# Performance work log

Measured on AMD Instinct MI355X. Metric: run time of the kernel, lower is better.

## Reference

```python
import jax, jax.numpy as jnp
import numpy as np
from jax import lax

B, C, W, H, K = 4, 32, 256, 256, 9
CENTER = K // 2
EXTEND = 1.0
EPS = 1e-5


def conv2d(x, w, b, stride=(1, 1), padding='SAME'):
    y = lax.conv_general_dilated(x, w, stride, padding,
                                 dimension_numbers=('NCHW', 'OIHW', 'NCHW'))
    return y + b[None, :, None, None]


def group_norm(x, scale, bias, groups):
    b, c, h, w = x.shape
    xg = x.reshape(b, groups, c // groups, h, w)
    mu = xg.mean(axis=(2, 3, 4), keepdims=True)
    var = xg.var(axis=(2, 3, 4), keepdims=True)
    xn = ((xg - mu) * lax.rsqrt(var + EPS)).reshape(b, c, h, w)
    return xn * scale[None, :, None, None] + bias[None, :, None, None]


def bilinear_sample(feat, py, px):
    # feat: (C, W, H); py, px: (W*K, H) pixel coords, already clamped in-range
    y0 = jnp.floor(py)
    x0 = jnp.floor(px)
    wy = py - y0
    wx = px - x0
    y0i = jnp.clip(y0, 0, W - 1).astype(jnp.int32)
    y1i = jnp.clip(y0 + 1, 0, W - 1).astype(jnp.int32)
    x0i = jnp.clip(x0, 0, H - 1).astype(jnp.int32)
    x1i = jnp.clip(x0 + 1, 0, H - 1).astype(jnp.int32)
    v00 = feat[:, y0i, x0i]
    v01 = feat[:, y0i, x1i]
    v10 = feat[:, y1i, x0i]
    v11 = feat[:, y1i, x1i]
    return (v00 * (1 - wy) * (1 - wx) + v01 * (1 - wy) * wx
            + v10 * wy * (1 - wx) + v11 * wy * wx)


def ds_conv(x, w_off, b_off, gn_off_scale, gn_off_bias, w_dsc, b_dsc, gn_scale, gn_bias):
    # offset branch: conv3x3 -> GroupNorm(K groups, 2K ch) -> tanh
    off = jnp.tanh(group_norm(conv2d(x, w_off, b_off), gn_off_scale, gn_off_bias, K))
    y_off = off[:, :K]  # (B, K, W, H); x-half of offsets unused when morph == 0
    # cumulative offset scan outward from center tap (center tap offset is 0)
    low = jnp.flip(jnp.cumsum(jnp.flip(y_off[:, :CENTER], 1), 1), 1)
    up = jnp.cumsum(y_off[:, CENTER + 1:], 1)
    y_cum = jnp.concatenate([low, jnp.zeros_like(y_off[:, :1]), up], axis=1)
    # coordinate maps (morph == 0: kernel spreads along x, offsets bend y)
    y_new = jnp.arange(W, dtype=x.dtype)[None, None, :, None] + y_cum * EXTEND
    x_new = (jnp.arange(H, dtype=x.dtype)[None, None, None, :]
             + jnp.linspace(-CENTER, CENTER, K, dtype=x.dtype)[None, :, None, None])
    x_new = jnp.broadcast_to(x_new, y_new.shape)
    gy = y_new.transpose(0, 2, 1, 3).reshape(-1, W * K, H)  # 'b k w h -> b (w k) h'
    gx = x_new.transpose(0, 2, 1, 3).reshape(-1, W * K, H)
    # normalize as torch grid_sample (align_corners=True) with clamp to [-1, 1]
    gy = jnp.clip(gy / W * 2 - 1, -1.0, 1.0)
    gx = jnp.clip(gx / H * 2 - 1, -1.0, 1.0)
    py = (gy + 1) * 0.5 * (W - 1)
    px = (gx + 1) * 0.5 * (H - 1)
    deformed = jax.vmap(bilinear_sample)(x, py, px)  # (B, C, W*K, H)
    out = conv2d(deformed, w_dsc, b_dsc, stride=(K, 1), padding='VALID')  # (B, C, W, H)
    out = group_norm(out, gn_scale, gn_bias, C // 4)
    return jax.nn.relu(out)


def setup_inputs() -> dict:
    key = jax.random.key(0)
    ks = jax.random.split(key, 3)
    return {
        'input': jax.random.normal(ks[0], (B, C, W, H), jnp.float32),
        'w_off': jax.random.normal(ks[1], (2 * K, C, 3, 3), jnp.float32) * 0.05,
        'b_off': jnp.zeros((2 * K,), jnp.float32),
        'gn_off_scale': jnp.ones((2 * K,), jnp.float32),
        'gn_off_bias': jnp.zeros((2 * K,), jnp.float32),
        'w_dsc': jax.random.normal(ks[2], (C, C, K, 1), jnp.float32) * 0.05,
        'b_dsc': jnp.zeros((C,), jnp.float32),
        'gn_scale': jnp.ones((C,), jnp.float32),
        'gn_bias': jnp.zeros((C,), jnp.float32),
    }


def reference(input, w_off, b_off, gn_off_scale, gn_off_bias, w_dsc, b_dsc, gn_scale, gn_bias):
    # in_channels == out_channels so input_adjust is Identity
    return ds_conv(input, w_off, b_off, gn_off_scale, gn_off_bias, w_dsc, b_dsc, gn_scale, gn_bias)
```

## Files before the change

### kernel.cpp

```cpp
#include <hip/hip_runtime.h>
#include <hip/hip_bf16.h>

#define BB 4
#define CC 32
#define WW 256
#define HH 256
#define WH (WW*HH)

typedef __attribute__((ext_vector_type(8))) short bf16x8;
typedef __attribute__((ext_vector_type(4))) short bf16x4;
typedef __attribute__((ext_vector_type(4))) float f32x4;

__device__ __forceinline__ short f2bf(float x) {
    union { float f; unsigned u; } a; a.f = x;
    unsigned r = (a.u + 0x7FFF + ((a.u >> 16) & 1)) >> 16;
    return (short)r;
}

__global__ void k0_init(const float* __restrict__ w_dsc, const float* __restrict__ w_off,
                        unsigned short* __restrict__ B3f, unsigned short* __restrict__ B8f,
                        unsigned short* __restrict__ B1f, unsigned short* __restrict__ B18f,
                        float* __restrict__ stats1, float* __restrict__ stats2) {
    int i = blockIdx.x * 256 + threadIdx.x;
    if (i < 8192) {
        int j = i & 7, l = (i >> 3) & 63, nt = (i >> 9) & 1, ch = i >> 10;
        int o = nt * 16 + (l & 15);
        int kl = ((l >> 4) << 3) | j;
        int tap = kl >> 2, cl = kl & 3;
        B3f[i] = (unsigned short)f2bf(w_dsc[(o * 32 + ch * 4 + cl) * 9 + tap]);
    } else if (i < 9216) {
        int e = i - 8192;
        int j = e & 7, l = (e >> 3) & 63, nt = e >> 9;
        int o = nt * 16 + (l & 15);
        int k8 = ((l >> 4) << 3) | j;
        B8f[e] = (unsigned short)f2bf(w_dsc[(o * 32 + k8) * 9 + 8]);
    } else if (i < 13312) {
        int e = i - 9216;
        int j = e & 7, l = (e >> 3) & 63, ch = e >> 9;
        int o = l & 15;
        int kl = ((l >> 4) << 3) | j;
        int tap = kl >> 2, cl = kl & 3;
        B1f[e] = (o < 10) ? (unsigned short)f2bf(w_off[(o * 32 + ch * 4 + cl) * 9 + tap]) : 0;
    } else if (i < 13824) {
        int e = i - 13312;
        int j = e & 7, l = (e >> 3) & 63;
        int o = l & 15;
        int k8 = ((l >> 4) << 3) | j;
        B18f[e] = (o < 10) ? (unsigned short)f2bf(w_off[(o * 32 + k8) * 9 + 8]) : 0;
    }
    if (i < 40) stats1[i] = 0.f;
    if (i < 64) stats2[i] = 0.f;
}

__global__ __launch_bounds__(256, 2) void k1_conv(
    const float* __restrict__ x, const unsigned short* __restrict__ B1f,
    const unsigned short* __restrict__ B18f, const float* __restrict__ b_off,
    float* __restrict__ off_buf, float* __restrict__ stats1) {
    __shared__ __align__(16) unsigned short tbf[8 * 4 * 136 * 4];
    __shared__ float scr[40];
    __shared__ __align__(16) short Apan[16 * 64 * 8];
    __shared__ __align__(16) short A8pan[16 * 64 * 8];

    const int b = blockIdx.z;
    const int w0 = blockIdx.y * 2;
    const int h0 = blockIdx.x * 128;
    const int p = threadIdx.x;
    const int lane = p & 63;
    const int wv = p >> 6;
    const int hl = p & 127;
    const int wi = p >> 7;
    const int mt = p >> 4;
    const int mrow = p & 15;

    const float* xb = x + (size_t)b * CC * WH;

#pragma unroll
    for (int u = 0; u < 5; ++u) {
        if (u < 4 || p < 64) {
            int s = p + u * 256;
            int g = s / 136;
            int rem = s - g * 136;
            int r = rem / 34;
            int k = rem - r * 34;
            int y = w0 - 1 + r;
            int g0 = h0 - 4 + (k << 2);
            f32x4 v0 = {0.f,0.f,0.f,0.f}, v1 = v0, v2 = v0, v3 = v0;
            if (y >= 0 && y < 256 && g0 >= 0 && g0 <= 252) {
                const float* bp2 = xb + y * 256 + g0;
                v0 = *(const f32x4*)(bp2 + (size_t)(g * 4 + 0) * WH);
                v1 = *(const f32x4*)(bp2 + (size_t)(g * 4 + 1) * WH);
                v2 = *(const f32x4*)(bp2 + (size_t)(g * 4 + 2) * WH);
                v3 = *(const f32x4*)(bp2 + (size_t)(g * 4 + 3) * WH);
            }
            int base = ((g * 4 + r) * 136 + (k << 2)) * 4;
#pragma unroll
            for (int i = 0; i < 4; ++i) {
                bf16x4 pv;
                pv[0] = f2bf(v0[i]); pv[1] = f2bf(v1[i]);
                pv[2] = f2bf(v2[i]); pv[3] = f2bf(v3[i]);
                *(bf16x4*)&tbf[base + i * 4] = pv;
            }
        }
    }

    bf16x8 Bf[8], B8g;
    {
        const bf16x8* bp = (const bf16x8*)B1f;
#pragma unroll
        for (int ch = 0; ch < 8; ++ch) Bf[ch] = bp[ch * 64 + lane];
        B8g = ((const bf16x8*)B18f)[lane];
    }

    f32x4 acc[4];
#pragma unroll
    for (int i = 0; i < 4; ++i) acc[i] = (f32x4){0.f, 0.f, 0.f, 0.f};

    __syncthreads();

#pragma unroll
    for (int ch = 0; ch < 8; ++ch) {
#pragma unroll
        for (int kg = 0; kg < 4; ++kg) {
            bf16x4 lo, hi;
            {
                int tap = kg * 2, dy = tap / 3, dx = tap - dy * 3;
                lo = *(const bf16x4*)&tbf[((ch * 4 + wi + dy) * 136 + hl + dx + 3) * 4];
            }
            {
                int tap = kg * 2 + 1, dy = tap / 3, dx = tap - dy * 3;
                hi = *(const bf16x4*)&tbf[((ch * 4 + wi + dy) * 136 + hl + dx + 3) * 4];
            }
            bf16x8 pv;
#pragma unroll
            for (int e = 0; e < 4; ++e) { pv[e] = lo[e]; pv[4 + e] = hi[e]; }
            *(bf16x8*)&Apan[mt * 512 + (kg * 16 + mrow) * 8] = pv;
        }
        {
            bf16x4 pv8 = *(const bf16x4*)&tbf[((ch * 4 + wi + 2) * 136 + hl + 5) * 4];
            *(bf16x4*)&A8pan[mt * 512 + ((ch >> 1) * 16 + mrow) * 8 + (ch & 1) * 4] = pv8;
        }
        __syncthreads();

#pragma unroll
        for (int i = 0; i < 4; ++i) {
            bf16x8 a = *(const bf16x8*)&Apan[((wv * 4 + i) * 64 + lane) * 8];
            acc[i] = __builtin_amdgcn_mfma_f32_16x16x32_bf16(a, Bf[ch], acc[i], 0, 0, 0);
        }
        __syncthreads();
    }
#pragma unroll
    for (int i = 0; i < 4; ++i) {
        bf16x8 a = *(const bf16x8*)&A8pan[((wv * 4 + i) * 64 + lane) * 8];
        acc[i] = __builtin_amdgcn_mfma_f32_16x16x32_bf16(a, B8g, acc[i], 0, 0, 0);
    }

    const int oc = lane & 15;
    float bias = (oc < 10) ? b_off[oc] : 0.f;
#pragma unroll
    for (int i = 0; i < 4; ++i)
#pragma unroll
        for (int r = 0; r < 4; ++r) acc[i][r] += bias;

    if (oc < 10) {
#pragma unroll
        for (int i = 0; i < 4; ++i) {
            int px = (wv * 4 + i) * 16 + (lane >> 4) * 4;
            size_t addr = (size_t)(b * 10 + oc) * WH +
                          (size_t)(w0 + (px >> 7)) * 256 + h0 + (px & 127);
            *(f32x4*)&off_buf[addr] = acc[i];
        }
    }

    float s = 0.f, q = 0.f;
#pragma unroll
    for (int i = 0; i < 4; ++i)
#pragma unroll
        for (int r = 0; r < 4; ++r) { float v = acc[i][r]; s += v; q += v * v; }
    s += __shfl_xor(s, 1, 64);  q += __shfl_xor(q, 1, 64);
    s += __shfl_xor(s, 16, 64); q += __shfl_xor(q, 16, 64);
    s += __shfl_xor(s, 32, 64); q += __shfl_xor(q, 32, 64);
    __syncthreads();
    if (lane < 10 && !(lane & 1)) {
        int g = lane >> 1;
        scr[(g * 2 + 0) * 4 + wv] = s;
        scr[(g * 2 + 1) * 4 + wv] = q;
    }
    __syncthreads();
    if (threadIdx.x < 10) {
        int g = threadIdx.x >> 1, which = threadIdx.x & 1;
        float sum = scr[(g * 2 + which) * 4 + 0] + scr[(g * 2 + which) * 4 + 1] +
                    scr[(g * 2 + which) * 4 + 2] + scr[(g * 2 + which) * 4 + 3];
        atomicAdd(&stats1[(b * 5 + g) * 2 + which], sum);
    }
}

__global__ __launch_bounds__(256, 2) void k3_sample(
    const float* __restrict__ xin, const float* __restrict__ off_buf,
    const float* __restrict__ stats1, const float* __restrict__ go_scale,
    const float* __restrict__ go_bias, const unsigned short* __restrict__ B3f,
    const unsigned short* __restrict__ B8f, const float* __restrict__ b_dsc,
    float* __restrict__ pre_out, float* __restrict__ stats2) {
    __shared__ float tile[4 * 14 * 96];
    __shared__ short Apan[16 * 64 * 8];
    __shared__ short A8pan[16 * 64 * 8];

    const int b = blockIdx.z;
    const int w0 = blockIdx.y * 4;
    const int h0 = blockIdx.x * 64;
    const int p = threadIdx.x;
    const int lane = p & 63;
    const int wv = p >> 6;
    const int h = h0 + (p & 63);
    const int w = w0 + (p >> 6);
    const int mt = p >> 4;
    const int mrow = p & 15;
    const int row0 = w0 - 5;
    const int col0 = h0 - 8;

    bf16x8 Bf[8][2], B8g[2];
    {
        const bf16x8* bp = (const bf16x8*)B3f;
#pragma unroll
        for (int ch = 0; ch < 8; ++ch) {
            Bf[ch][0] = bp[(ch * 2 + 0) * 64 + lane];
            Bf[ch][1] = bp[(ch * 2 + 1) * 64 + lane];
        }
        B8g[0] = ((const bf16x8*)B8f)[lane];
        B8g[1] = ((const bf16x8*)B8f)[64 + lane];
    }

    const float INV1 = 1.f / (2.f * WH);
    float t9[9];
    size_t obase = (size_t)b * 10 * WH + (size_t)w * 256 + h;
#pragma unroll
    for (int c = 0; c < 9; ++c) {
        float v = off_buf[obase + (size_t)c * WH];
        int g = c >> 1;
        float s1 = stats1[(b * 5 + g) * 2 + 0];
        float q1 = stats1[(b * 5 + g) * 2 + 1];
        float mean = s1 * INV1;
        float istd = rsqrtf(fmaf(q1, INV1, -(mean * mean)) + 1e-5f);
        v = (v - mean) * istd * go_scale[c] + go_bias[c];
        t9[c] = tanhf(v);
    }
    float ycum[9];
    ycum[3] = t9[3];
    ycum[2] = ycum[3] + t9[2];
    ycum[1] = ycum[2] + t9[1];
    ycum[0] = ycum[1] + t9[0];
    ycum[4] = 0.f;
    ycum[5] = t9[5];
    ycum[6] = ycum[5] + t9[6];
    ycum[7] = ycum[6] + t9[7];
    ycum[8] = ycum[7] + t9[8];

    f32x4 acc[4][2];
#pragma unroll
    for (int i = 0; i < 4; ++i) {
        acc[i][0] = (f32x4){0.f, 0.f, 0.f, 0.f};
        acc[i][1] = (f32x4){0.f, 0.f, 0.f, 0.f};
    }

    const float* xb = xin + (size_t)b * CC * WH;
    const float SC = 255.f / 256.f;

#pragma unroll
    for (int ch = 0; ch < 8; ++ch) {
        for (int t = threadIdx.x; t < 1064; t += 256) {
            int c = t / 266;
            int rem = t - c * 266;
            int r = rem / 19;
            int cf = rem - r * 19;
            int y = min(max(row0 + r, 0), 255);
            int g0 = col0 + (cf << 2);
            const float* src = xb + (size_t)(ch * 4 + c) * WH + y * 256;
            float4 val;
            if (g0 >= 0 && g0 <= 252) {
                val = *(const float4*)(src + g0);
            } else {
                val.x = src[min(max(g0, 0), 255)];
                val.y = src[min(max(g0 + 1, 0), 255)];
                val.z = src[min(max(g0 + 2, 0), 255)];
                val.w = src[min(max(g0 + 3, 0), 255)];
            }
            *(float4*)(tile + (c * 14 + r) * 96 + (cf << 2)) = val;
        }
        __syncthreads();

#pragma unroll
        for (int kg = 0; kg < 4; ++kg) {
            bf16x8 pv;
#pragma unroll
            for (int t = 0; t < 2; ++t) {
                int k = kg * 2 + t;
                float py = fminf(fmaxf(((float)w + ycum[k]) * SC, 0.f), 255.f);
                float pxc = fminf(fmaxf((float)(h + k - 4) * SC, 0.f), 255.f);
                float y0f = floorf(py), x0f = floorf(pxc);
                float wy = py - y0f, wx = pxc - x0f;
                int r0 = (int)y0f - row0;
                int r1 = min((int)y0f + 1, 255) - row0;
                int tc = (int)x0f - col0;
                float w00 = (1.f - wy) * (1.f - wx);
                float w01 = (1.f - wy) * wx;
                float w10 = wy * (1.f - wx);
                float w11 = wy * wx;
#pragma unroll
                for (int cl = 0; cl < 4; ++cl) {
                    const float* p0 = tile + (cl * 14 + r0) * 96 + tc;
                    const float* p1 = tile + (cl * 14 + r1) * 96 + tc;
                    float v = fmaf(w00, p0[0],
                              fmaf(w01, p0[1], fmaf(w10, p1[0], w11 * p1[1])));
                    pv[t * 4 + cl] = f2bf(v);
                }
            }
            *(bf16x8*)&Apan[mt * 512 + (kg * 16 + mrow) * 8] = pv;
        }
        {
            float py = fminf(fmaxf(((float)w + ycum[8]) * SC, 0.f), 255.f);
            float pxc = fminf(fmaxf((float)(h + 4) * SC, 0.f), 255.f);
            float y0f = floorf(py), x0f = floorf(pxc);
            float wy = py - y0f, wx = pxc - x0f;
            int r0 = (int)y0f - row0;
            int r1 = min((int)y0f + 1, 255) - row0;
            int tc = (int)x0f - col0;
            float w00 = (1.f - wy) * (1.f - wx);
            float w01 = (1.f - wy) * wx;
            float w10 = wy * (1.f - wx);
            float w11 = wy * wx;
            bf16x4 pv8;
#pragma unroll
            for (int cl = 0; cl < 4; ++cl) {
                const float* p0 = tile + (cl * 14 + r0) * 96 + tc;
                const float* p1 = tile + (cl * 14 + r1) * 96 + tc;
                float v = fmaf(w00, p0[0],
                          fmaf(w01, p0[1], fmaf(w10, p1[0], w11 * p1[1])));
                pv8[cl] = f2bf(v);
            }
            *(bf16x4*)&A8pan[mt * 512 + ((ch >> 1) * 16 + mrow) * 8 + (ch & 1) * 4] = pv8;
        }
        __syncthreads();

#pragma unroll
        for (int i = 0; i < 4; ++i) {
            bf16x8 a = *(const bf16x8*)&Apan[((wv * 4 + i) * 64 + lane) * 8];
            acc[i][0] = __builtin_amdgcn_mfma_f32_16x16x32_bf16(a, Bf[ch][0], acc[i][0], 0, 0, 0);
            acc[i][1] = __builtin_amdgcn_mfma_f32_16x16x32_bf16(a, Bf[ch][1], acc[i][1], 0, 0, 0);
        }
    }
#pragma unroll
    for (int i = 0; i < 4; ++i) {
        bf16x8 a = *(const bf16x8*)&A8pan[((wv * 4 + i) * 64 + lane) * 8];
        acc[i][0] = __builtin_amdgcn_mfma_f32_16x16x32_bf16(a, B8g[0], acc[i][0], 0, 0, 0);
        acc[i][1] = __builtin_amdgcn_mfma_f32_16x16x32_bf16(a, B8g[1], acc[i][1], 0, 0, 0);
    }

    const int oc0 = lane & 15;
    float bias0 = b_dsc[oc0];
    float bias1 = b_dsc[16 + oc0];
#pragma unroll
    for (int i = 0; i < 4; ++i)
#pragma unroll
        for (int r = 0; r < 4; ++r) { acc[i][0][r] += bias0; acc[i][1][r] += bias1; }

#pragma unroll
    for (int i = 0; i < 4; ++i) {
        int px = (wv * 4 + i) * 16 + (lane >> 4) * 4;
        size_t rowoff = (size_t)(w0 + (px >> 6)) * 256 + h0 + (px & 63);
        *(f32x4*)&pre_out[(size_t)(b * 32 + oc0) * WH + rowoff] = acc[i][0];
        *(f32x4*)&pre_out[(size_t)(b * 32 + 16 + oc0) * WH + rowoff] = acc[i][1];
    }

    float s0 = 0.f, q0 = 0.f, s1 = 0.f, q1 = 0.f;
#pragma unroll
    for (int i = 0; i < 4; ++i)
#pragma unroll
        for (int r = 0; r < 4; ++r) {
            float v0 = acc[i][0][r], v1 = acc[i][1][r];
            s0 += v0; q0 += v0 * v0; s1 += v1; q1 += v1 * v1;
        }
#pragma unroll
    for (int m = 0; m < 4; ++m) {
        int d = (m == 0) ? 1 : (m == 1) ? 2 : (m == 2) ? 16 : 32;
        s0 += __shfl_xor(s0, d, 64); q0 += __shfl_xor(q0, d, 64);
        s1 += __shfl_xor(s1, d, 64); q1 += __shfl_xor(q1, d, 64);
    }
    __syncthreads();
    float* scratch = tile;
    if (lane < 16 && !(lane & 3)) {
        int g = lane >> 2;
        scratch[((0 * 4 + g) * 2 + 0) * 4 + wv] = s0;
        scratch[((0 * 4 + g) * 2 + 1) * 4 + wv] = q0;
        scratch[((1 * 4 + g) * 2 + 0) * 4 + wv] = s1;
        scratch[((1 * 4 + g) * 2 + 1) * 4 + wv] = q1;
    }
    __syncthreads();
    if (threadIdx.x < 16) {
        int gg = threadIdx.x >> 1, which = threadIdx.x & 1;
        float sum = scratch[(gg * 2 + which) * 4 + 0] + scratch[(gg * 2 + which) * 4 + 1] +
                    scratch[(gg * 2 + which) * 4 + 2] + scratch[(gg * 2 + which) * 4 + 3];
        atomicAdd(&stats2[(b * 8 + gg) * 2 + which], sum);
    }
}

__global__ __launch_bounds__(256) void k5_gn(float4* __restrict__ out,
                                             const float* __restrict__ stats2,
                                             const float* __restrict__ gs,
                                             const float* __restrict__ gb) {
    int idx = blockIdx.x * 256 + threadIdx.x;
    int bo = idx >> 14;
    int b = bo >> 5;
    int o = bo & 31;
    int g = o >> 2;
    const float INV2 = 1.f / (4.f * WH);
    float s = stats2[(b * 8 + g) * 2 + 0];
    float q = stats2[(b * 8 + g) * 2 + 1];
    float mean = s * INV2;
    float istd = rsqrtf(fmaf(q, INV2, -(mean * mean)) + 1e-5f);
    float sc = gs[o] * istd;
    float bi = gb[o] - mean * sc;
    float4 v = out[idx];
    v.x = fmaxf(fmaf(v.x, sc, bi), 0.f);
    v.y = fmaxf(fmaf(v.y, sc, bi), 0.f);
    v.z = fmaxf(fmaf(v.z, sc, bi), 0.f);
    v.w = fmaxf(fmaf(v.w, sc, bi), 0.f);
    out[idx] = v;
}

extern "C" void kernel_launch(void* const* d_in, const int* in_sizes, int n_in,
                              void* d_out, int out_size, void* d_ws, size_t ws_size,
                              hipStream_t stream) {
    const float* x        = (const float*)d_in[0];
    const float* w_off    = (const float*)d_in[1];
    const float* b_off    = (const float*)d_in[2];
    const float* go_scale = (const float*)d_in[3];
    const float* go_bias  = (const float*)d_in[4];
    const float* w_dsc    = (const float*)d_in[5];
    const float* b_dsc    = (const float*)d_in[6];
    const float* gn_scale = (const float*)d_in[7];
    const float* gn_bias  = (const float*)d_in[8];
    float* out = (float*)d_out;

    float* ws = (float*)d_ws;
    float* off_buf = ws;
    unsigned short* B3f  = (unsigned short*)(ws + 2621440);
    unsigned short* B8f  = (unsigned short*)(ws + 2625536);
    unsigned short* B1f  = (unsigned short*)(ws + 2626048);
    unsigned short* B18f = (unsigned short*)(ws + 2628096);
    float* stats1 = ws + 2628352;
    float* stats2 = stats1 + 80;

    k0_init<<<54, 256, 0, stream>>>(w_dsc, w_off, B3f, B8f, B1f, B18f, stats1, stats2);
    k1_conv<<<dim3(2, 128, BB), 256, 0, stream>>>(x, B1f, B18f, b_off, off_buf, stats1);
    k3_sample<<<dim3(4, 64, BB), 256, 0, stream>>>(x, off_buf, stats1, go_scale, go_bias,
                                                   B3f, B8f, b_dsc, out, stats2);
    k5_gn<<<8192, 256, 0, stream>>>((float4*)out, stats2, gn_scale, gn_bias);
}
```

Baseline: 206.2 us.

## Double-buffer input tile with async global-to-LDS loads prefetching next channel group

The input tile in shared memory becomes two buffers. It is filled with `__builtin_amdgcn_global_load_lds` direct-to-LDS loads instead of register-staged float4 copies. The load for the next channel group is issued before bilinear sampling and MFMA on the current group, so global latency overlaps compute. Border handling now clamps whole 16-byte vectors, which is only safe because edge columns are never read. LDS use roughly grows by another tile, which may limit occupancy.

```diff
diff --git a/kernel.cpp b/kernel.cpp
--- a/kernel.cpp
+++ b/kernel.cpp
@@ -10,6 +10,9 @@
 typedef __attribute__((ext_vector_type(8))) short bf16x8;
 typedef __attribute__((ext_vector_type(4))) short bf16x4;
 typedef __attribute__((ext_vector_type(4))) float f32x4;
+
+typedef __attribute__((address_space(1))) const void gvoid;
+typedef __attribute__((address_space(3))) void lvoid;
 
 __device__ __forceinline__ short f2bf(float x) {
     union { float f; unsigned u; } a; a.f = x;
@@ -200,9 +203,9 @@
     const float* __restrict__ go_bias, const unsigned short* __restrict__ B3f,
     const unsigned short* __restrict__ B8f, const float* __restrict__ b_dsc,
     float* __restrict__ pre_out, float* __restrict__ stats2) {
-    __shared__ float tile[4 * 14 * 96];
-    __shared__ short Apan[16 * 64 * 8];
-    __shared__ short A8pan[16 * 64 * 8];
+    __shared__ __align__(16) float tile[2][4 * 14 * 96];
+    __shared__ __align__(16) short Apan[16 * 64 * 8];
+    __shared__ __align__(16) short A8pan[16 * 64 * 8];
 
     const int b = blockIdx.z;
     const int w0 = blockIdx.y * 4;
@@ -217,6 +220,28 @@
     const int row0 = w0 - 5;
     const int col0 = h0 - 8;
 
+    const float* xb = xin + (size_t)b * CC * WH;
+
+    auto dma = [&](int buf, int chn) {
+#pragma unroll
+        for (int u = 0; u < 6; ++u) {
+            if (u < 5 || p < 64) {
+                int t = p + u * 256;
+                int c = t / 336;
+                int rem = t - c * 336;
+                int r = rem / 24;
+                int cf4 = rem - r * 24;
+                int y = min(max(row0 + r, 0), 255);
+                int g0 = min(max(col0 + (cf4 << 2), 0), 252);
+                const float* gp = xb + (size_t)(chn * 4 + c) * WH + y * 256 + g0;
+                __builtin_amdgcn_global_load_lds((gvoid*)gp,
+                                                 (lvoid*)&tile[buf][t * 4], 16, 0, 0);
+            }
+        }
+    };
+
+    dma(0, 0);
+
     bf16x8 Bf[8][2], B8g[2];
     {
         const bf16x8* bp = (const bf16x8*)B3f;
@@ -261,31 +286,16 @@
         acc[i][1] = (f32x4){0.f, 0.f, 0.f, 0.f};
     }
 
-    const float* xb = xin + (size_t)b * CC * WH;
     const float SC = 255.f / 256.f;
 
 #pragma unroll
     for (int ch = 0; ch < 8; ++ch) {
-        for (int t = threadIdx.x; t < 1064; t += 256) {
-            int c = t / 266;
-            int rem = t - c * 266;
-            int r = rem / 19;
-            int cf = rem - r * 19;
-            int y = min(max(row0 + r, 0), 255);
-            int g0 = col0 + (cf << 2);
-            const float* src = xb + (size_t)(ch * 4 + c) * WH + y * 256;
-            float4 val;
-            if (g0 >= 0 && g0 <= 252) {
-                val = *(const float4*)(src + g0);
-            } else {
-                val.x = src[min(max(g0, 0), 255)];
-                val.y = src[min(max(g0 + 1, 0), 255)];
-                val.z = src[min(max(g0 + 2, 0), 255)];
-                val.w = src[min(max(g0 + 3, 0), 255)];
-            }
-            *(float4*)(tile + (c * 14 + r) * 96 + (cf << 2)) = val;
-        }
+        asm volatile("s_waitcnt vmcnt(0)" ::: "memory");
+        __builtin_amdgcn_sched_barrier(0);
         __syncthreads();
+        __builtin_amdgcn_sched_barrier(0);
+        if (ch < 7) dma((ch + 1) & 1, ch + 1);
+        const float* tb = tile[ch & 1];
 
 #pragma unroll
         for (int kg = 0; kg < 4; ++kg) {
@@ -306,8 +316,8 @@
                 float w11 = wy * wx;
 #pragma unroll
                 for (int cl = 0; cl < 4; ++cl) {
-                    const float* p0 = tile + (cl * 14 + r0) * 96 + tc;
-                    const float* p1 = tile + (cl * 14 + r1) * 96 + tc;
+                    const float* p0 = tb + (cl * 14 + r0) * 96 + tc;
+                    const float* p1 = tb + (cl * 14 + r1) * 96 + tc;
                     float v = fmaf(w00, p0[0],
                               fmaf(w01, p0[1], fmaf(w10, p1[0], w11 * p1[1])));
                     pv[t * 4 + cl] = f2bf(v);
@@ -330,8 +340,8 @@
             bf16x4 pv8;
 #pragma unroll
             for (int cl = 0; cl < 4; ++cl) {
-                const float* p0 = tile + (cl * 14 + r0) * 96 + tc;
-                const float* p1 = tile + (cl * 14 + r1) * 96 + tc;
+                const float* p0 = tb + (cl * 14 + r0) * 96 + tc;
+                const float* p1 = tb + (cl * 14 + r1) * 96 + tc;
                 float v = fmaf(w00, p0[0],
                           fmaf(w01, p0[1], fmaf(w10, p1[0], w11 * p1[1])));
                 pv8[cl] = f2bf(v);
@@ -385,7 +395,7 @@
         s1 += __shfl_xor(s1, d, 64); q1 += __shfl_xor(q1, d, 64);
     }
     __syncthreads();
-    float* scratch = tile;
+    float* scratch = tile[0];
     if (lane < 16 && !(lane & 3)) {
         int g = lane >> 2;
         scratch[((0 * 4 + g) * 2 + 0) * 4 + wv] = s0;
```

Result: faster. 183.2 us (-11.2%).
